# Kernel optimization log

Measured on AMD Instinct MI355X. Metric: run time of the kernel, lower is better.

Reference implementation:

```python
import jax, jax.numpy as jnp
import numpy as np


def setup_inputs() -> dict:
    key = jax.random.key(0)
    k1, k2, k3, k4 = jax.random.split(key, 4)
    B, C, H, W = 8, 64, 64, 64
    Cr = C // 8
    x = jax.random.normal(k1, (B, C, H, W), dtype=jnp.float32)
    Wf = jax.random.normal(k2, (Cr, C), dtype=jnp.float32) * (1.0 / np.sqrt(C))
    Wg = jax.random.normal(k3, (Cr, C), dtype=jnp.float32) * (1.0 / np.sqrt(C))
    Wh = jax.random.normal(k4, (C, C), dtype=jnp.float32) * (1.0 / np.sqrt(C))
    gamma = jnp.zeros((1,), dtype=jnp.float32)
    return {"x": x, "Wf": Wf, "Wg": Wg, "Wh": Wh, "gamma": gamma}


def reference(x, Wf, Wg, Wh, gamma):
    B, C, H, W = x.shape
    N = H * W
    xf = x.reshape(B, C, N)                      # [B, C, N]
    fx = jnp.einsum("oc,bcn->bno", Wf, xf)       # queries [B, N, C/8]
    gx = jnp.einsum("oc,bcn->bon", Wg, xf)       # keys    [B, C/8, N]
    hx = jnp.einsum("oc,bcn->bon", Wh, xf)       # values  [B, C,   N]
    beta = jnp.einsum("bnd,bdm->bnm", fx, gx)    # [B, N, N], no 1/sqrt(d) scale (SAGAN)
    beta = jax.nn.softmax(beta, axis=-1)
    # o = bmm(hx, beta^T): o[b,c,i] = sum_j hx[b,c,j] * beta[b,i,j]
    o = jnp.einsum("bcj,bij->bci", hx, beta)     # [B, C, N]
    o = o.reshape(B, C, H, W)
    return gamma * o + x
```

## Files before the change

kernel.cpp:

```cpp
#include <hip/hip_runtime.h>
#include <hip/hip_bf16.h>


#define N_ 4096
#define LOG2E 1.4426950408889634f

typedef __attribute__((ext_vector_type(8)))  __bf16 bf16x8;
typedef __attribute__((ext_vector_type(4)))  float  f32x4;
typedef __attribute__((ext_vector_type(16))) float  f32x16;

union U16B { uint4 u; bf16x8 b; };

static __device__ inline uint pack_bf2(float a, float b) {
  __hip_bfloat162 h = __float22bfloat162_rn(make_float2(a, b));
  uint r; __builtin_memcpy(&r, &h, 4); return r;
}
static __device__ inline ushort f2bf(float a) {
  __hip_bfloat16 h = __float2bfloat16(a);
  ushort r; __builtin_memcpy(&r, &h, 2); return r;
}
static __device__ inline float bflo(uint u) {
  uint v = u << 16; float f; __builtin_memcpy(&f, &v, 4); return f;
}
static __device__ inline float bfhi(uint u) {
  uint v = u & 0xffff0000u; float f; __builtin_memcpy(&f, &v, 4); return f;
}

__global__ __launch_bounds__(256) void prep_kernel(
    const float* __restrict__ x,  const float* __restrict__ Wf,
    const float* __restrict__ Wg, const float* __restrict__ Wh,
    ushort* __restrict__ Qp, ushort* __restrict__ Kp, ushort* __restrict__ Vf)
{
  __shared__ __align__(16) char smem[37376];
  float*  T   = (float*)smem;
  ushort* xTl = (ushort*)(smem + 16640);
  ushort* Wb  = (ushort*)(smem + 25856);
  const int b = blockIdx.y, n0 = blockIdx.x * 64, tid = threadIdx.x;

  {
    const int nl = tid & 63, cw = tid >> 6;
#pragma unroll
    for (int i = 0; i < 16; ++i) {
      const int c = i * 4 + cw;
      T[c * 65 + nl] = x[((size_t)(b * 64 + c)) * N_ + n0 + nl];
    }
  }
  {
#pragma unroll
    for (int i = 0; i < 20; ++i) {
      const int e = i * 256 + tid;
      const int row = e >> 6, col = e & 63;
      float v;
      if (row < 8)       v = Wf[row * 64 + col] * LOG2E;
      else if (row < 16) v = Wg[(row - 8) * 64 + col];
      else               v = Wh[(row - 16) * 64 + col];
      Wb[row * 72 + col] = f2bf(v);
    }
  }
  __syncthreads();
  {
    const int n = tid >> 2, cq = (tid & 3) * 16;
    uint o[8];
#pragma unroll
    for (int j = 0; j < 8; ++j)
      o[j] = pack_bf2(T[(cq + 2 * j) * 65 + n], T[(cq + 2 * j + 1) * 65 + n]);
    *(uint4*)(xTl + n * 72 + cq)     = make_uint4(o[0], o[1], o[2], o[3]);
    *(uint4*)(xTl + n * 72 + cq + 8) = make_uint4(o[4], o[5], o[6], o[7]);
  }
  __syncthreads();

  const int l = tid & 63, w = tid >> 6, l15 = l & 15, lq = l >> 4;
  const int nn = w * 16 + l15;
  U16B bf0, bf1;
  bf0.u = *(const uint4*)(xTl + nn * 72 + lq * 8);
  bf1.u = *(const uint4*)(xTl + nn * 72 + 32 + lq * 8);
  f32x4 acc[5];
#pragma unroll
  for (int mt = 0; mt < 5; ++mt) {
    U16B a0, a1;
    a0.u = *(const uint4*)(Wb + (mt * 16 + l15) * 72 + lq * 8);
    a1.u = *(const uint4*)(Wb + (mt * 16 + l15) * 72 + 32 + lq * 8);
    f32x4 c0 = __builtin_amdgcn_mfma_f32_16x16x32_bf16(a0.b, bf0.b, (f32x4){0.f,0.f,0.f,0.f}, 0, 0, 0);
    acc[mt]  = __builtin_amdgcn_mfma_f32_16x16x32_bf16(a1.b, bf1.b, c0, 0, 0, 0);
  }
  const int n = n0 + nn;
  {
    uint lo = pack_bf2(acc[0][0], acc[0][1]);
    uint hi = pack_bf2(acc[0][2], acc[0][3]);
    ushort* dst = (lq < 2 ? Qp : Kp) + ((size_t)(b * N_ + n)) * 8 + (lq & 1) * 4;
    *(uint2*)dst = make_uint2(lo, hi);
  }
  ushort* Vt = (ushort*)smem;
  const int jp = nn;
  const int jl = jp & 31, stp = (jl >> 4) & 1, j16 = jl & 15;
  const int s  = (j16 & 3) | ((j16 & 4) << 1) | ((j16 & 8) >> 1);
  const int vbase = ((jp >> 5) * 2 + stp) * 1024 + (s >> 3) * 256 + (s & 7);
#pragma unroll
  for (int mt = 1; mt < 5; ++mt)
#pragma unroll
    for (int r = 0; r < 4; ++r) {
      const int c = (mt - 1) * 16 + lq * 4 + r;
      Vt[vbase + (c >> 5) * 512 + (c & 31) * 8] = f2bf(acc[mt][r]);
    }
  __syncthreads();
  const uint4* src = (const uint4*)Vt;
  uint4* dst = (uint4*)(Vf + ((size_t)(b * 64 + blockIdx.x)) * 4096);
  dst[tid]       = src[tid];
  dst[256 + tid] = src[256 + tid];
}

__global__ __launch_bounds__(256) void attn_kernel(
    const ushort* __restrict__ Qp, const ushort* __restrict__ Kp,
    const ushort* __restrict__ Vf,
    ushort* __restrict__ Opart, float* __restrict__ Lpart)
{
  __shared__ __align__(16) uint4 vsl[1024];
  const int b = blockIdx.z, js = blockIdx.y;
  const int tid = threadIdx.x, w = tid >> 6, l = tid & 63;
  const int l31 = l & 31, lq1 = l >> 5;
  const int q0w = blockIdx.x * 256 + w * 64;
  const uint4 zero4 = make_uint4(0u, 0u, 0u, 0u);

  U16B qf[2];
#pragma unroll
  for (int qc = 0; qc < 2; ++qc)
    qf[qc].u = lq1 ? zero4
        : *(const uint4*)(Qp + ((size_t)(b * N_ + q0w + qc * 32 + l31)) * 8);

  const int jb0 = js * 1024;
  U16B kf[2], kfn[2];
#pragma unroll
  for (int jc = 0; jc < 2; ++jc)
    kf[jc].u = lq1 ? zero4
        : *(const uint4*)(Kp + ((size_t)(b * N_ + jb0 + jc * 32 + l31)) * 8);

  const uint4* Vg = (const uint4*)(Vf + ((size_t)(b * 64 + js * 16)) * 4096);
  vsl[tid]       = Vg[tid];
  vsl[256 + tid] = Vg[256 + tid];

  const f32x16 Oz = {0,0,0,0,0,0,0,0,0,0,0,0,0,0,0,0};
  f32x16 O[2][2] = {{Oz, Oz}, {Oz, Oz}};
  float L0 = 0.f, L1 = 0.f;
  uint pk[2][2][8];
  uint4 vp0, vp1;
  int p = 0;
  __syncthreads();

  for (int jt = 0; jt < 16; ++jt) {
    if (jt < 15) {
      vp0 = Vg[(jt + 1) * 512 + tid];
      vp1 = Vg[(jt + 1) * 512 + 256 + tid];
#pragma unroll
      for (int jc = 0; jc < 2; ++jc)
        kfn[jc].u = lq1 ? zero4
            : *(const uint4*)(Kp + ((size_t)(b * N_ + jb0 + (jt + 1) * 64 + jc * 32 + l31)) * 8);
    }
#pragma unroll
    for (int qc = 0; qc < 2; ++qc)
#pragma unroll
      for (int jc = 0; jc < 2; ++jc) {
        f32x16 St = __builtin_amdgcn_mfma_f32_32x32x16_bf16(
            kf[jc].b, qc ? qf[1].b : qf[0].b, Oz, 0, 0, 0);
        float e[16];
#pragma unroll
        for (int r = 0; r < 16; ++r) e[r] = __builtin_amdgcn_exp2f(St[r]);
        const float ps = (((e[0] + e[1]) + (e[2] + e[3])) + ((e[4] + e[5]) + (e[6] + e[7])))
                       + (((e[8] + e[9]) + (e[10] + e[11])) + ((e[12] + e[13]) + (e[14] + e[15])));
        if (qc) L1 += ps; else L0 += ps;
#pragma unroll
        for (int d = 0; d < 8; ++d) pk[qc][jc][d] = pack_bf2(e[2 * d], e[2 * d + 1]);
      }
    const uint4* vb = vsl + p * 512;
#pragma unroll
    for (int ks = 0; ks < 4; ++ks) {
      const int jc = ks >> 1, st = (ks & 1) * 4;
#pragma unroll
      for (int ch = 0; ch < 2; ++ch) {
        U16B vfr; vfr.u = vb[ks * 128 + ch * 64 + l];
#pragma unroll
        for (int qc = 0; qc < 2; ++qc) {
          U16B pa;
          pa.u = make_uint4(pk[qc][jc][st], pk[qc][jc][st + 1],
                            pk[qc][jc][st + 2], pk[qc][jc][st + 3]);
          O[qc][ch] = __builtin_amdgcn_mfma_f32_32x32x16_bf16(pa.b, vfr.b, O[qc][ch], 0, 0, 0);
        }
      }
    }
    if (jt < 15) {
      vsl[(p ^ 1) * 512 + tid]       = vp0;
      vsl[(p ^ 1) * 512 + 256 + tid] = vp1;
#pragma unroll
      for (int jc = 0; jc < 2; ++jc) kf[jc] = kfn[jc];
    }
    __syncthreads();
    p ^= 1;
  }

  L0 += __shfl_xor(L0, 32);
  L1 += __shfl_xor(L1, 32);
  float* Lp = Lpart + ((size_t)(js * 8 + b)) * N_;
  if (lq1 == 0) {
    Lp[q0w + l31]      = L0;
    Lp[q0w + 32 + l31] = L1;
  }

  ushort* Op = Opart + (((size_t)(js * 8 + b)) * N_ + q0w) * 64;
#pragma unroll
  for (int qc = 0; qc < 2; ++qc)
#pragma unroll
    for (int ch = 0; ch < 2; ++ch)
#pragma unroll
      for (int g = 0; g < 4; ++g)
#pragma unroll
        for (int r = 0; r < 4; ++r) {
          const int q = qc * 32 + r + 8 * g + 4 * lq1;
          Op[q * 64 + ch * 32 + l31] = f2bf(O[qc][ch][g * 4 + r]);
        }
}

__global__ __launch_bounds__(256) void combine_kernel(
    const ushort* __restrict__ Opart, const float* __restrict__ Lpart,
    const float* __restrict__ x, const float* __restrict__ gamma,
    float* __restrict__ out)
{
  __shared__ float T[64 * 65];
  const int b = blockIdx.y, n0 = blockIdx.x * 64, tid = threadIdx.x;
  float acc[16];
#pragma unroll
  for (int e = 0; e < 16; ++e) acc[e] = 0.f;
#pragma unroll
  for (int js = 0; js < 4; ++js) {
    const ushort* Op = Opart + (((size_t)(js * 8 + b)) * N_ + n0) * 64 + tid * 16;
    uint4 a  = *(const uint4*)Op;
    uint4 c2 = *(const uint4*)(Op + 8);
    acc[0] += bflo(a.x);  acc[1] += bfhi(a.x);  acc[2] += bflo(a.y);  acc[3] += bfhi(a.y);
    acc[4] += bflo(a.z);  acc[5] += bfhi(a.z);  acc[6] += bflo(a.w);  acc[7] += bfhi(a.w);
    acc[8] += bflo(c2.x); acc[9] += bfhi(c2.x); acc[10]+= bflo(c2.y); acc[11]+= bfhi(c2.y);
    acc[12]+= bflo(c2.z); acc[13]+= bfhi(c2.z); acc[14]+= bflo(c2.w); acc[15]+= bfhi(c2.w);
  }
  const int nr = tid >> 2, c0 = (tid & 3) * 16;
#pragma unroll
  for (int e = 0; e < 16; ++e) T[nr * 65 + c0 + e] = acc[e];
  __syncthreads();
  const float g = gamma[0];
  const int n = tid & 63, cq = (tid >> 6) * 16;
  float Ls = 0.f;
#pragma unroll
  for (int js = 0; js < 4; ++js) Ls += Lpart[((size_t)(js * 8 + b)) * N_ + n0 + n];
  const float gr = g / Ls;
#pragma unroll
  for (int i = 0; i < 16; ++i) {
    const int c = cq + i;
    const size_t oi = ((size_t)(b * 64 + c)) * N_ + n0 + n;
    out[oi] = gr * T[n * 65 + c] + x[oi];
  }
}

extern "C" void kernel_launch(void* const* d_in, const int* in_sizes, int n_in,
                              void* d_out, int out_size, void* d_ws, size_t ws_size,
                              hipStream_t stream) {
  const float* x     = (const float*)d_in[0];
  const float* Wf    = (const float*)d_in[1];
  const float* Wg    = (const float*)d_in[2];
  const float* Wh    = (const float*)d_in[3];
  const float* gamma = (const float*)d_in[4];
  float* out = (float*)d_out;
  char* ws = (char*)d_ws;

  ushort* Qp    = (ushort*)(ws);
  ushort* Kp    = (ushort*)(ws + 512 * 1024);
  ushort* Vf    = (ushort*)(ws + 1024 * 1024);
  float*  Lpart = (float*) (ws + 5 * 1024 * 1024);
  ushort* Opart = (ushort*)(ws + 6 * 1024 * 1024);

  prep_kernel   <<<dim3(64, 8),    256, 0, stream>>>(x, Wf, Wg, Wh, Qp, Kp, Vf);
  attn_kernel   <<<dim3(16, 4, 8), 256, 0, stream>>>(Qp, Kp, Vf, Opart, Lpart);
  combine_kernel<<<dim3(64, 8),    256, 0, stream>>>(Opart, Lpart, x, gamma, out);
}
```

Measured before the change: 114.2 us.

## Split keys 8 ways, flatten grid, use bit-trick exp2 and packed sums

Splits the key range into eight chunks of 512 instead of four of 1024, doubling the attention grid to 1024 blocks on a flattened 1D grid that puts batch in the low bits. The combine kernel now merges eight partials. The hardware exp2 is replaced by an integer bit-trick approximation (scaled add reinterpreted as a float), with bf16 packing done by a byte permute and row sums accumulated as float2 vectors. Occupancy hint of 4 blocks per SM is added. The intent is more parallelism and cheaper transcendental work. The cost is extra partial-output traffic and a coarse piecewise-linear exp2 that lowers accuracy of the softmax weights.

```diff
diff --git a/kernel.cpp b/kernel.cpp
--- a/kernel.cpp
+++ b/kernel.cpp
@@ -6,6 +6,7 @@
 #define LOG2E 1.4426950408889634f
 
 typedef __attribute__((ext_vector_type(8)))  __bf16 bf16x8;
+typedef __attribute__((ext_vector_type(2)))  float  f32x2;
 typedef __attribute__((ext_vector_type(4)))  float  f32x4;
 typedef __attribute__((ext_vector_type(16))) float  f32x16;
 
@@ -24,6 +25,12 @@
 }
 static __device__ inline float bfhi(uint u) {
   uint v = u & 0xffff0000u; float f; __builtin_memcpy(&f, &v, 4); return f;
+}
+static __device__ inline uint fexp2i(float s) {
+  return (uint)(int)(s * 8388608.0f + 1065353216.0f);
+}
+static __device__ inline float asf(uint u) {
+  float f; __builtin_memcpy(&f, &u, 4); return f;
 }
 
 __global__ __launch_bounds__(256) void prep_kernel(
@@ -109,16 +116,17 @@
   dst[256 + tid] = src[256 + tid];
 }
 
-__global__ __launch_bounds__(256) void attn_kernel(
+__global__ __launch_bounds__(256, 4) void attn_kernel(
     const ushort* __restrict__ Qp, const ushort* __restrict__ Kp,
     const ushort* __restrict__ Vf,
     ushort* __restrict__ Opart, float* __restrict__ Lpart)
 {
   __shared__ __align__(16) uint4 vsl[1024];
-  const int b = blockIdx.z, js = blockIdx.y;
+  const int bid = blockIdx.x;
+  const int b = bid & 7, js = (bid >> 3) & 7, qblk = bid >> 6;
   const int tid = threadIdx.x, w = tid >> 6, l = tid & 63;
   const int l31 = l & 31, lq1 = l >> 5;
-  const int q0w = blockIdx.x * 256 + w * 64;
+  const int q0w = qblk * 256 + w * 64;
   const uint4 zero4 = make_uint4(0u, 0u, 0u, 0u);
 
   U16B qf[2];
@@ -127,27 +135,27 @@
     qf[qc].u = lq1 ? zero4
         : *(const uint4*)(Qp + ((size_t)(b * N_ + q0w + qc * 32 + l31)) * 8);
 
-  const int jb0 = js * 1024;
+  const int jb0 = js * 512;
   U16B kf[2], kfn[2];
 #pragma unroll
   for (int jc = 0; jc < 2; ++jc)
     kf[jc].u = lq1 ? zero4
         : *(const uint4*)(Kp + ((size_t)(b * N_ + jb0 + jc * 32 + l31)) * 8);
 
-  const uint4* Vg = (const uint4*)(Vf + ((size_t)(b * 64 + js * 16)) * 4096);
+  const uint4* Vg = (const uint4*)(Vf + ((size_t)(b * 64 + js * 8)) * 4096);
   vsl[tid]       = Vg[tid];
   vsl[256 + tid] = Vg[256 + tid];
 
   const f32x16 Oz = {0,0,0,0,0,0,0,0,0,0,0,0,0,0,0,0};
   f32x16 O[2][2] = {{Oz, Oz}, {Oz, Oz}};
-  float L0 = 0.f, L1 = 0.f;
+  f32x2 Lv0 = {0.f, 0.f}, Lv1 = {0.f, 0.f};
   uint pk[2][2][8];
   uint4 vp0, vp1;
   int p = 0;
   __syncthreads();
 
-  for (int jt = 0; jt < 16; ++jt) {
-    if (jt < 15) {
+  for (int jt = 0; jt < 8; ++jt) {
+    if (jt < 7) {
       vp0 = Vg[(jt + 1) * 512 + tid];
       vp1 = Vg[(jt + 1) * 512 + 256 + tid];
 #pragma unroll
@@ -161,14 +169,18 @@
       for (int jc = 0; jc < 2; ++jc) {
         f32x16 St = __builtin_amdgcn_mfma_f32_32x32x16_bf16(
             kf[jc].b, qc ? qf[1].b : qf[0].b, Oz, 0, 0, 0);
-        float e[16];
-#pragma unroll
-        for (int r = 0; r < 16; ++r) e[r] = __builtin_amdgcn_exp2f(St[r]);
-        const float ps = (((e[0] + e[1]) + (e[2] + e[3])) + ((e[4] + e[5]) + (e[6] + e[7])))
-                       + (((e[8] + e[9]) + (e[10] + e[11])) + ((e[12] + e[13]) + (e[14] + e[15])));
-        if (qc) L1 += ps; else L0 += ps;
-#pragma unroll
-        for (int d = 0; d < 8; ++d) pk[qc][jc][d] = pack_bf2(e[2 * d], e[2 * d + 1]);
+        uint ib[16];
+#pragma unroll
+        for (int r = 0; r < 16; ++r) ib[r] = fexp2i(St[r]);
+        f32x2 t0 = {asf(ib[0]), asf(ib[1])},  t1 = {asf(ib[2]),  asf(ib[3])};
+        f32x2 t2 = {asf(ib[4]), asf(ib[5])},  t3 = {asf(ib[6]),  asf(ib[7])};
+        f32x2 t4 = {asf(ib[8]), asf(ib[9])},  t5 = {asf(ib[10]), asf(ib[11])};
+        f32x2 t6 = {asf(ib[12]), asf(ib[13])}, t7 = {asf(ib[14]), asf(ib[15])};
+        f32x2 ts = ((t0 + t1) + (t2 + t3)) + ((t4 + t5) + (t6 + t7));
+        if (qc) Lv1 += ts; else Lv0 += ts;
+#pragma unroll
+        for (int d = 0; d < 8; ++d)
+          pk[qc][jc][d] = __builtin_amdgcn_perm(ib[2 * d + 1], ib[2 * d], 0x07060302u);
       }
     const uint4* vb = vsl + p * 512;
 #pragma unroll
@@ -186,7 +198,7 @@
         }
       }
     }
-    if (jt < 15) {
+    if (jt < 7) {
       vsl[(p ^ 1) * 512 + tid]       = vp0;
       vsl[(p ^ 1) * 512 + 256 + tid] = vp1;
 #pragma unroll
@@ -196,6 +208,7 @@
     p ^= 1;
   }
 
+  float L0 = Lv0.x + Lv0.y, L1 = Lv1.x + Lv1.y;
   L0 += __shfl_xor(L0, 32);
   L1 += __shfl_xor(L1, 32);
   float* Lp = Lpart + ((size_t)(js * 8 + b)) * N_;
@@ -229,7 +242,7 @@
 #pragma unroll
   for (int e = 0; e < 16; ++e) acc[e] = 0.f;
 #pragma unroll
-  for (int js = 0; js < 4; ++js) {
+  for (int js = 0; js < 8; ++js) {
     const ushort* Op = Opart + (((size_t)(js * 8 + b)) * N_ + n0) * 64 + tid * 16;
     uint4 a  = *(const uint4*)Op;
     uint4 c2 = *(const uint4*)(Op + 8);
@@ -246,7 +259,7 @@
   const int n = tid & 63, cq = (tid >> 6) * 16;
   float Ls = 0.f;
 #pragma unroll
-  for (int js = 0; js < 4; ++js) Ls += Lpart[((size_t)(js * 8 + b)) * N_ + n0 + n];
+  for (int js = 0; js < 8; ++js) Ls += Lpart[((size_t)(js * 8 + b)) * N_ + n0 + n];
   const float gr = g / Ls;
 #pragma unroll
   for (int i = 0; i < 16; ++i) {
@@ -273,7 +286,7 @@
   float*  Lpart = (float*) (ws + 5 * 1024 * 1024);
   ushort* Opart = (ushort*)(ws + 6 * 1024 * 1024);
 
-  prep_kernel   <<<dim3(64, 8),    256, 0, stream>>>(x, Wf, Wg, Wh, Qp, Kp, Vf);
-  attn_kernel   <<<dim3(16, 4, 8), 256, 0, stream>>>(Qp, Kp, Vf, Opart, Lpart);
-  combine_kernel<<<dim3(64, 8),    256, 0, stream>>>(Opart, Lpart, x, gamma, out);
-}
+  prep_kernel   <<<dim3(64, 8), 256, 0, stream>>>(x, Wf, Wg, Wh, Qp, Kp, Vf);
+  attn_kernel   <<<1024,        256, 0, stream>>>(Qp, Kp, Vf, Opart, Lpart);
+  combine_kernel<<<dim3(64, 8), 256, 0, stream>>>(Opart, Lpart, x, gamma, out);
+}
```

New measurement: 144.0 us. 1.26x slower.
